# Kernel optimization log

Hardware: AMD Instinct MI355X
Metric: run time of the kernel (lower is better)

## Reference

```python
import jax, jax.numpy as jnp
import numpy as np

B, T, N_X, N_U, N_Y, H = 2048, 2048, 4, 2, 1, 64
MIN_X = jnp.array([0.0, 0.0, 0.0, -jnp.inf], dtype=jnp.float32)
MAX_X = jnp.array([10.0, 10.0, 10.0, jnp.inf], dtype=jnp.float32)
MIN_Y = jnp.array([0.0], dtype=jnp.float32)
MAX_Y = jnp.array([10.0], dtype=jnp.float32)


def setup_inputs() -> dict:
    key = jax.random.key(0)
    ks = jax.random.split(key, 6)
    return {
        "x_0": jax.random.uniform(ks[0], (B, N_X), dtype=jnp.float32) * 5.0,
        "u": jax.random.normal(ks[1], (B, T, N_U), dtype=jnp.float32),
        "theta_f": jnp.array([0.1925, 0.2429, 0.1697, 0.0444, 0.1642], dtype=jnp.float32),
        "theta_h": jnp.zeros((1,), dtype=jnp.float32),
        "tau_u": jnp.ones((1,), dtype=jnp.float32),
        "tau_y": jnp.ones((1,), dtype=jnp.float32),
        "W1": jax.random.normal(ks[2], (N_X + N_U + 5, H), dtype=jnp.float32) / np.sqrt(N_X + N_U + 5),
        "b1": jnp.zeros((H,), dtype=jnp.float32),
        "W2": jax.random.normal(ks[3], (H, N_X), dtype=jnp.float32) * 0.05,
        "Wh": jax.random.normal(ks[4], (N_X, N_Y), dtype=jnp.float32),
    }


def reference(x_0, u, theta_f, theta_h, tau_u, tau_y, W1, b1, W2, Wh):
    Bc = x_0.shape[0]
    tf = jnp.broadcast_to(theta_f[None, :], (Bc, theta_f.shape[0]))
    scale = tau_u[0] / tau_y[0]

    def f(x, ut):
        feat = jnp.concatenate([x, ut, tf], axis=-1)  # (B, n_x+n_u+5)
        return jnp.tanh(feat @ W1 + b1) @ W2 * scale  # (B, n_x)

    def h(x):
        return x @ Wh + theta_h  # (B, n_y)

    y0 = h(x_0)  # unclamped initial output, as in the torch loop

    def step(carry, ut):
        x_step, y_step = carry
        dx = f(x_step, ut)
        x_raw = x_step + dx
        y_new = jnp.clip(h(x_raw), MIN_Y, MAX_Y)  # y computed from pre-clamp state
        x_new = jnp.clip(x_raw, MIN_X, MAX_X)
        return (x_new, y_new), (x_step, y_step)

    u_t = jnp.moveaxis(u, 1, 0)  # (T, B, n_u)
    _, (xs, ys) = jax.lax.scan(step, (x_0, y0), u_t)
    x = jnp.moveaxis(xs, 0, 1)  # (B, T, n_x)
    y = jnp.moveaxis(ys, 0, 1)  # (B, T, n_y)
    return (x, y)
```

## Files before the change

kernel.cpp:

```cpp
#include <hip/hip_runtime.h>

#define B_SZ 2048
#define T_SZ 2048

using f32x16 = float __attribute__((ext_vector_type(16)));
using f32x2  = float __attribute__((ext_vector_type(2)));

template<int CTRL>
__device__ __forceinline__ float dppf(float v) {
  int r = __builtin_amdgcn_update_dpp(0, __builtin_bit_cast(int, v), CTRL, 0xf, 0xf, true);
  return __builtin_bit_cast(float, r);
}

__device__ __forceinline__ f32x2 pkfma(f32x2 a, f32x2 b, f32x2 c) {
  return __builtin_elementwise_fma(a, b, c);
}

#define SSTR 264
#define SBUF (8 * SSTR)

__global__ __launch_bounds__(256, 1) void sss_kernel(
    const float* __restrict__ x0p, const float* __restrict__ up,
    const float* __restrict__ tfp, const float* __restrict__ thp,
    const float* __restrict__ tup, const float* __restrict__ typ,
    const float* __restrict__ W1p, const float* __restrict__ b1p,
    const float* __restrict__ W2p, const float* __restrict__ Whp,
    float* __restrict__ outp)
{
  __shared__ float stageF[2 * SBUF];

  const int tid  = threadIdx.x;
  const int lane = tid & 63;
  const int wv   = __builtin_amdgcn_readfirstlane((int)(tid >> 6));
  const int grp  = lane >> 4;
  const int sl   = lane & 15;
  const int k    = lane & 3;
  const int b0   = blockIdx.x * 16 + wv * 4;
  const int b    = b0 + grp;

  const float K = 2.8853900817779268f;
  f32x2 w1_01[6], w1_23[6];
#pragma unroll
  for (int r = 0; r < 6; ++r) {
    w1_01[r] = f32x2{W1p[r * 64 + sl]      * K, W1p[r * 64 + sl + 16] * K};
    w1_23[r] = f32x2{W1p[r * 64 + sl + 32] * K, W1p[r * 64 + sl + 48] * K};
  }
  float ccs[4];
#pragma unroll
  for (int i = 0; i < 4; ++i) {
    const int u = sl + 16 * i;
    float t = b1p[u];
#pragma unroll
    for (int q = 0; q < 5; ++q) t = fmaf(tfp[q], W1p[(6 + q) * 64 + u], t);
    ccs[i] = t * K;
  }
  const f32x2 cc01 = f32x2{ccs[0], ccs[1]};
  const f32x2 cc23 = f32x2{ccs[2], ccs[3]};

  const float scale = tup[0] / typ[0];
  f32x2 wAB[4], wCD[4];
#pragma unroll
  for (int i = 0; i < 4; ++i) {
    const float4 w2r = ((const float4*)W2p)[sl + 16 * i];
    float col[4] = {w2r.x * scale, w2r.y * scale, w2r.z * scale, w2r.w * scale};
    wAB[i] = f32x2{col[k], col[k ^ 1]};
    wCD[i] = f32x2{col[k ^ 2], col[k ^ 3]};
  }

  const float whl = Whp[k];
  const float th  = thp[0];

  const float lo = (k == 3) ? -__builtin_inff() : 0.0f;
  const float hi = (k == 3) ?  __builtin_inff() : 10.0f;

  float xlane = x0p[b * 4 + k];
  float x0v = dppf<0x00>(xlane);
  float x1v = dppf<0x55>(xlane);
  float x2v = dppf<0xAA>(xlane);
  float x3v = dppf<0xFF>(xlane);

  float p0 = xlane * whl;
  p0 += dppf<0xB1>(p0);
  p0 += dppf<0x4E>(p0);
  float yv = p0 + th;

  const bool is4 = (sl == 4);

  const int m   = sl;
  const int xr  = lane >> 4;
  const int t0  = m >> 1;
  const int k0  = (2 * m) & 3;
  const int rdoff = t0 * SSTR + wv * 64 + 16 * xr + k0;
  const int yoff  = (lane & 7) * SSTR + wv * 64 + 16 * (lane >> 3) + 4;
  float2* gxp = (float2*)outp + (size_t)(b0 + (lane >> 4)) * (T_SZ * 2) + (lane & 15);
  float*  gyp = outp + (size_t)B_SZ * T_SZ * 4 + (size_t)(b0 + (lane >> 3)) * T_SZ + (lane & 7);

  const f32x16* up16 = (const f32x16*)(up + (size_t)b * (T_SZ * 2));
  f32x16 uch = up16[0];
  const int NC = T_SZ / 8;

  for (int c = 0; c < NC; ++c) {
    const int g = (c + 1 < NC) ? c + 1 : NC - 1;
    const f32x16 unx = up16[g];
    float* sw = &stageF[(c & 1) * SBUF + tid];
#pragma unroll
    for (int jj = 0; jj < 8; ++jj) {
      const float vdata = is4 ? yv : xlane;
      sw[jj * SSTR] = vdata;

      const float u0 = uch[2 * jj];
      const float u1 = uch[2 * jj + 1];
      const f32x2 u0p = f32x2{u0, u0};
      const f32x2 u1p = f32x2{u1, u1};

      const f32x2 b01 = pkfma(u1p, w1_01[5], pkfma(u0p, w1_01[4], cc01));
      const f32x2 b23 = pkfma(u1p, w1_23[5], pkfma(u0p, w1_23[4], cc23));

      const f32x2 x0s = f32x2{x0v, x0v};
      const f32x2 x1s = f32x2{x1v, x1v};
      const f32x2 x2s = f32x2{x2v, x2v};
      const f32x2 x3s = f32x2{x3v, x3v};
      const f32x2 mA01 = pkfma(x1s, w1_01[1], x0s * w1_01[0]);
      const f32x2 mB01 = pkfma(x3s, w1_01[3], x2s * w1_01[2]);
      const f32x2 a01  = (b01 + mA01) + mB01;
      const f32x2 mA23 = pkfma(x1s, w1_23[1], x0s * w1_23[0]);
      const f32x2 mB23 = pkfma(x3s, w1_23[3], x2s * w1_23[2]);
      const f32x2 a23  = (b23 + mA23) + mB23;

      float h[4];
      {
        const float av[4] = {a01[0], a01[1], a23[0], a23[1]};
#pragma unroll
        for (int i = 0; i < 4; ++i) {
          const float e  = __builtin_amdgcn_exp2f(av[i]);
          const float rr = __builtin_amdgcn_rcpf(e + 1.0f);
          h[i] = fmaf(-2.0f, rr, 1.0f);
        }
      }
      const f32x2 h0s = f32x2{h[0], h[0]};
      const f32x2 h1s = f32x2{h[1], h[1]};
      const f32x2 h2s = f32x2{h[2], h[2]};
      const f32x2 h3s = f32x2{h[3], h[3]};

      f32x2 qAB = h0s * wAB[0];
      qAB = pkfma(h1s, wAB[1], qAB);
      qAB = pkfma(h2s, wAB[2], qAB);
      qAB = pkfma(h3s, wAB[3], qAB);
      f32x2 qCD = h0s * wCD[0];
      qCD = pkfma(h1s, wCD[1], qCD);
      qCD = pkfma(h2s, wCD[2], qCD);
      qCD = pkfma(h3s, wCD[3], qCD);

      float v = (qAB[0] + dppf<0xB1>(qAB[1]))
              + (dppf<0x4E>(qCD[0]) + dppf<0x1B>(qCD[1]));
      v += dppf<0x124>(v);
      v += dppf<0x128>(v);

      const float w = xlane + v;
      xlane = __builtin_amdgcn_fmed3f(w, lo, hi);

      float p = w * whl;
      p += dppf<0xB1>(p);
      p += dppf<0x4E>(p);
      yv = __builtin_amdgcn_fmed3f(p + th, 0.0f, 10.0f);

      x0v = dppf<0x00>(xlane);
      x1v = dppf<0x55>(xlane);
      x2v = dppf<0xAA>(xlane);
      x3v = dppf<0xFF>(xlane);
    }
    {
      const int bb = (c & 1) * SBUF;
      const float2 xv = *(const float2*)&stageF[bb + rdoff];
      *gxp = xv;
      if (lane < 32) {
        const float yy = stageF[bb + yoff];
        *gyp = yy;
      }
      gxp += 16;
      gyp += 8;
    }
    uch = unx;
  }
}

extern "C" void kernel_launch(void* const* d_in, const int* in_sizes, int n_in,
                              void* d_out, int out_size, void* d_ws, size_t ws_size,
                              hipStream_t stream) {
  (void)in_sizes; (void)n_in; (void)out_size; (void)d_ws; (void)ws_size;
  sss_kernel<<<dim3(B_SZ / 16), dim3(256), 0, stream>>>(
      (const float*)d_in[0], (const float*)d_in[1], (const float*)d_in[2],
      (const float*)d_in[3], (const float*)d_in[4], (const float*)d_in[5],
      (const float*)d_in[6], (const float*)d_in[7], (const float*)d_in[8],
      (const float*)d_in[9], (float*)d_out);
}
```

Baseline: 340.9 us.

## Interleave two batch recurrences per wave and fold tanh constant into state

Each wave now advances two independent batch rows in lockstep so the serial dependency chain of one row can overlap with the other, halving the grid size. The tanh expression is rewritten as 1-2r so the constant term from W2 is precomputed into an offset added to the state, removing per-step multiply-adds, and the cross-lane reduction uses a tree form. The cost is higher register pressure, doubled shared staging, and fewer blocks, which may leave CUs with less wave-level parallelism.

```diff
diff --git a/kernel.cpp b/kernel.cpp
--- a/kernel.cpp
+++ b/kernel.cpp
@@ -27,7 +27,7 @@
     const float* __restrict__ W2p, const float* __restrict__ Whp,
     float* __restrict__ outp)
 {
-  __shared__ float stageF[2 * SBUF];
+  __shared__ float stageF[4 * SBUF];
 
   const int tid  = threadIdx.x;
   const int lane = tid & 63;
@@ -35,8 +35,9 @@
   const int grp  = lane >> 4;
   const int sl   = lane & 15;
   const int k    = lane & 3;
-  const int b0   = blockIdx.x * 16 + wv * 4;
-  const int b    = b0 + grp;
+  const int b0   = blockIdx.x * 32 + wv * 8;
+  const int bA   = b0 + grp;
+  const int bB   = b0 + 4 + grp;
 
   const float K = 2.8853900817779268f;
   f32x2 w1_01[6], w1_23[6];
@@ -67,22 +68,31 @@
     wCD[i] = f32x2{col[k ^ 2], col[k ^ 3]};
   }
 
+  {
+  }
+  const f32x2 oAB = (wAB[0] + wAB[1]) + (wAB[2] + wAB[3]);
+  const f32x2 oCD = (wCD[0] + wCD[1]) + (wCD[2] + wCD[3]);
+  float Cq = (oAB[0] + dppf<0xB1>(oAB[1])) + (dppf<0x4E>(oCD[0]) + dppf<0x1B>(oCD[1]));
+  const float Ck = (Cq + dppf<0x124>(Cq)) + (dppf<0x128>(Cq) + dppf<0x12C>(Cq));
+
   const float whl = Whp[k];
   const float th  = thp[0];
-
   const float lo = (k == 3) ? -__builtin_inff() : 0.0f;
   const float hi = (k == 3) ?  __builtin_inff() : 10.0f;
 
-  float xlane = x0p[b * 4 + k];
-  float x0v = dppf<0x00>(xlane);
-  float x1v = dppf<0x55>(xlane);
-  float x2v = dppf<0xAA>(xlane);
-  float x3v = dppf<0xFF>(xlane);
-
-  float p0 = xlane * whl;
-  p0 += dppf<0xB1>(p0);
-  p0 += dppf<0x4E>(p0);
-  float yv = p0 + th;
+  float xlaneA = x0p[bA * 4 + k];
+  float x0vA = dppf<0x00>(xlaneA), x1vA = dppf<0x55>(xlaneA);
+  float x2vA = dppf<0xAA>(xlaneA), x3vA = dppf<0xFF>(xlaneA);
+  float xCA = xlaneA + Ck;
+  float pA0 = xlaneA * whl; pA0 += dppf<0xB1>(pA0); pA0 += dppf<0x4E>(pA0);
+  float yvA = pA0 + th;
+
+  float xlaneB = x0p[bB * 4 + k];
+  float x0vB = dppf<0x00>(xlaneB), x1vB = dppf<0x55>(xlaneB);
+  float x2vB = dppf<0xAA>(xlaneB), x3vB = dppf<0xFF>(xlaneB);
+  float xCB = xlaneB + Ck;
+  float pB0 = xlaneB * whl; pB0 += dppf<0xB1>(pB0); pB0 += dppf<0x4E>(pB0);
+  float yvB = pB0 + th;
 
   const bool is4 = (sl == 4);
 
@@ -92,95 +102,118 @@
   const int k0  = (2 * m) & 3;
   const int rdoff = t0 * SSTR + wv * 64 + 16 * xr + k0;
   const int yoff  = (lane & 7) * SSTR + wv * 64 + 16 * (lane >> 3) + 4;
-  float2* gxp = (float2*)outp + (size_t)(b0 + (lane >> 4)) * (T_SZ * 2) + (lane & 15);
-  float*  gyp = outp + (size_t)B_SZ * T_SZ * 4 + (size_t)(b0 + (lane >> 3)) * T_SZ + (lane & 7);
-
-  const f32x16* up16 = (const f32x16*)(up + (size_t)b * (T_SZ * 2));
-  f32x16 uch = up16[0];
+  float2* gxpA = (float2*)outp + (size_t)(b0 + (lane >> 4)) * (T_SZ * 2) + (lane & 15);
+  float*  gypA = outp + (size_t)B_SZ * T_SZ * 4 + (size_t)(b0 + (lane >> 3)) * T_SZ + (lane & 7);
+  float2* gxpB = (float2*)outp + (size_t)(b0 + 4 + (lane >> 4)) * (T_SZ * 2) + (lane & 15);
+  float*  gypB = outp + (size_t)B_SZ * T_SZ * 4 + (size_t)(b0 + 4 + (lane >> 3)) * T_SZ + (lane & 7);
+
+  const f32x16* up16A = (const f32x16*)(up + (size_t)bA * (T_SZ * 2));
+  const f32x16* up16B = (const f32x16*)(up + (size_t)bB * (T_SZ * 2));
+  f32x16 uchA = up16A[0];
+  f32x16 uchB = up16B[0];
   const int NC = T_SZ / 8;
 
   for (int c = 0; c < NC; ++c) {
     const int g = (c + 1 < NC) ? c + 1 : NC - 1;
-    const f32x16 unx = up16[g];
-    float* sw = &stageF[(c & 1) * SBUF + tid];
+    const f32x16 unxA = up16A[g];
+    const f32x16 unxB = up16B[g];
+    float* swA = &stageF[((c & 1) * 2 + 0) * SBUF + tid];
+    float* swB = &stageF[((c & 1) * 2 + 1) * SBUF + tid];
 #pragma unroll
     for (int jj = 0; jj < 8; ++jj) {
-      const float vdata = is4 ? yv : xlane;
-      sw[jj * SSTR] = vdata;
-
-      const float u0 = uch[2 * jj];
-      const float u1 = uch[2 * jj + 1];
-      const f32x2 u0p = f32x2{u0, u0};
-      const f32x2 u1p = f32x2{u1, u1};
-
-      const f32x2 b01 = pkfma(u1p, w1_01[5], pkfma(u0p, w1_01[4], cc01));
-      const f32x2 b23 = pkfma(u1p, w1_23[5], pkfma(u0p, w1_23[4], cc23));
-
-      const f32x2 x0s = f32x2{x0v, x0v};
-      const f32x2 x1s = f32x2{x1v, x1v};
-      const f32x2 x2s = f32x2{x2v, x2v};
-      const f32x2 x3s = f32x2{x3v, x3v};
-      const f32x2 mA01 = pkfma(x1s, w1_01[1], x0s * w1_01[0]);
-      const f32x2 mB01 = pkfma(x3s, w1_01[3], x2s * w1_01[2]);
-      const f32x2 a01  = (b01 + mA01) + mB01;
-      const f32x2 mA23 = pkfma(x1s, w1_23[1], x0s * w1_23[0]);
-      const f32x2 mB23 = pkfma(x3s, w1_23[3], x2s * w1_23[2]);
-      const f32x2 a23  = (b23 + mA23) + mB23;
-
-      float h[4];
+      const float vdA = is4 ? yvA : xlaneA;
+      swA[jj * SSTR] = vdA;
+      const float vdB = is4 ? yvB : xlaneB;
+      swB[jj * SSTR] = vdB;
+
+      const float u0A = uchA[2 * jj], u1A = uchA[2 * jj + 1];
+      const float u0B = uchB[2 * jj], u1B = uchB[2 * jj + 1];
+      const f32x2 bA01 = pkfma(f32x2{u1A, u1A}, w1_01[5], pkfma(f32x2{u0A, u0A}, w1_01[4], cc01));
+      const f32x2 bB01 = pkfma(f32x2{u1B, u1B}, w1_01[5], pkfma(f32x2{u0B, u0B}, w1_01[4], cc01));
+      const f32x2 bA23 = pkfma(f32x2{u1A, u1A}, w1_23[5], pkfma(f32x2{u0A, u0A}, w1_23[4], cc23));
+      const f32x2 bB23 = pkfma(f32x2{u1B, u1B}, w1_23[5], pkfma(f32x2{u0B, u0B}, w1_23[4], cc23));
+
+      const f32x2 x0sA = f32x2{x0vA, x0vA}, x1sA = f32x2{x1vA, x1vA};
+      const f32x2 x2sA = f32x2{x2vA, x2vA}, x3sA = f32x2{x3vA, x3vA};
+      const f32x2 x0sB = f32x2{x0vB, x0vB}, x1sB = f32x2{x1vB, x1vB};
+      const f32x2 x2sB = f32x2{x2vB, x2vB}, x3sB = f32x2{x3vB, x3vB};
+      const f32x2 mA01A = pkfma(x1sA, w1_01[1], x0sA * w1_01[0]);
+      const f32x2 mA01B = pkfma(x1sB, w1_01[1], x0sB * w1_01[0]);
+      const f32x2 mB01A = pkfma(x3sA, w1_01[3], x2sA * w1_01[2]);
+      const f32x2 mB01B = pkfma(x3sB, w1_01[3], x2sB * w1_01[2]);
+      const f32x2 aA01 = (mA01A + mB01A) + bA01;
+      const f32x2 aB01 = (mA01B + mB01B) + bB01;
+      const f32x2 mA23A = pkfma(x1sA, w1_23[1], x0sA * w1_23[0]);
+      const f32x2 mA23B = pkfma(x1sB, w1_23[1], x0sB * w1_23[0]);
+      const f32x2 mB23A = pkfma(x3sA, w1_23[3], x2sA * w1_23[2]);
+      const f32x2 mB23B = pkfma(x3sB, w1_23[3], x2sB * w1_23[2]);
+      const f32x2 aA23 = (mA23A + mB23A) + bA23;
+      const f32x2 aB23 = (mA23B + mB23B) + bB23;
+
+      float rA[4], rB[4];
       {
-        const float av[4] = {a01[0], a01[1], a23[0], a23[1]};
+        const float avA[4] = {aA01[0], aA01[1], aA23[0], aA23[1]};
+        const float avB[4] = {aB01[0], aB01[1], aB23[0], aB23[1]};
 #pragma unroll
         for (int i = 0; i < 4; ++i) {
-          const float e  = __builtin_amdgcn_exp2f(av[i]);
-          const float rr = __builtin_amdgcn_rcpf(e + 1.0f);
-          h[i] = fmaf(-2.0f, rr, 1.0f);
+          const float eA = __builtin_amdgcn_exp2f(avA[i]);
+          const float eB = __builtin_amdgcn_exp2f(avB[i]);
+          rA[i] = __builtin_amdgcn_rcpf(eA + 1.0f);
+          rB[i] = __builtin_amdgcn_rcpf(eB + 1.0f);
         }
       }
-      const f32x2 h0s = f32x2{h[0], h[0]};
-      const f32x2 h1s = f32x2{h[1], h[1]};
-      const f32x2 h2s = f32x2{h[2], h[2]};
-      const f32x2 h3s = f32x2{h[3], h[3]};
-
-      f32x2 qAB = h0s * wAB[0];
-      qAB = pkfma(h1s, wAB[1], qAB);
-      qAB = pkfma(h2s, wAB[2], qAB);
-      qAB = pkfma(h3s, wAB[3], qAB);
-      f32x2 qCD = h0s * wCD[0];
-      qCD = pkfma(h1s, wCD[1], qCD);
-      qCD = pkfma(h2s, wCD[2], qCD);
-      qCD = pkfma(h3s, wCD[3], qCD);
-
-      float v = (qAB[0] + dppf<0xB1>(qAB[1]))
-              + (dppf<0x4E>(qCD[0]) + dppf<0x1B>(qCD[1]));
-      v += dppf<0x124>(v);
-      v += dppf<0x128>(v);
-
-      const float w = xlane + v;
-      xlane = __builtin_amdgcn_fmed3f(w, lo, hi);
-
-      float p = w * whl;
-      p += dppf<0xB1>(p);
-      p += dppf<0x4E>(p);
-      yv = __builtin_amdgcn_fmed3f(p + th, 0.0f, 10.0f);
-
-      x0v = dppf<0x00>(xlane);
-      x1v = dppf<0x55>(xlane);
-      x2v = dppf<0xAA>(xlane);
-      x3v = dppf<0xFF>(xlane);
+
+      const f32x2 qABA = pkfma(f32x2{rA[1], rA[1]}, wAB[1], f32x2{rA[0], rA[0]} * wAB[0])
+                       + pkfma(f32x2{rA[3], rA[3]}, wAB[3], f32x2{rA[2], rA[2]} * wAB[2]);
+      const f32x2 qABB = pkfma(f32x2{rB[1], rB[1]}, wAB[1], f32x2{rB[0], rB[0]} * wAB[0])
+                       + pkfma(f32x2{rB[3], rB[3]}, wAB[3], f32x2{rB[2], rB[2]} * wAB[2]);
+      const f32x2 qCDA = pkfma(f32x2{rA[1], rA[1]}, wCD[1], f32x2{rA[0], rA[0]} * wCD[0])
+                       + pkfma(f32x2{rA[3], rA[3]}, wCD[3], f32x2{rA[2], rA[2]} * wCD[2]);
+      const f32x2 qCDB = pkfma(f32x2{rB[1], rB[1]}, wCD[1], f32x2{rB[0], rB[0]} * wCD[0])
+                       + pkfma(f32x2{rB[3], rB[3]}, wCD[3], f32x2{rB[2], rB[2]} * wCD[2]);
+
+      const float vA = (qABA[0] + dppf<0xB1>(qABA[1]))
+                     + (dppf<0x4E>(qCDA[0]) + dppf<0x1B>(qCDA[1]));
+      const float vB = (qABB[0] + dppf<0xB1>(qABB[1]))
+                     + (dppf<0x4E>(qCDB[0]) + dppf<0x1B>(qCDB[1]));
+      const float VA = (vA + dppf<0x124>(vA)) + (dppf<0x128>(vA) + dppf<0x12C>(vA));
+      const float VB = (vB + dppf<0x124>(vB)) + (dppf<0x128>(vB) + dppf<0x12C>(vB));
+
+      const float wA = fmaf(-2.0f, VA, xCA);
+      const float wB = fmaf(-2.0f, VB, xCB);
+
+      float pA = wA * whl; pA += dppf<0xB1>(pA); pA += dppf<0x4E>(pA);
+      yvA = __builtin_amdgcn_fmed3f(pA + th, 0.0f, 10.0f);
+      float pB = wB * whl; pB += dppf<0xB1>(pB); pB += dppf<0x4E>(pB);
+      yvB = __builtin_amdgcn_fmed3f(pB + th, 0.0f, 10.0f);
+
+      xlaneA = __builtin_amdgcn_fmed3f(wA, lo, hi);
+      xlaneB = __builtin_amdgcn_fmed3f(wB, lo, hi);
+      xCA = xlaneA + Ck;
+      xCB = xlaneB + Ck;
+      x0vA = dppf<0x00>(xlaneA); x0vB = dppf<0x00>(xlaneB);
+      x1vA = dppf<0x55>(xlaneA); x1vB = dppf<0x55>(xlaneB);
+      x2vA = dppf<0xAA>(xlaneA); x2vB = dppf<0xAA>(xlaneB);
+      x3vA = dppf<0xFF>(xlaneA); x3vB = dppf<0xFF>(xlaneB);
     }
     {
-      const int bb = (c & 1) * SBUF;
-      const float2 xv = *(const float2*)&stageF[bb + rdoff];
-      *gxp = xv;
+      const int bbA = ((c & 1) * 2 + 0) * SBUF;
+      const int bbB = ((c & 1) * 2 + 1) * SBUF;
+      const float2 xvA = *(const float2*)&stageF[bbA + rdoff];
+      const float2 xvB = *(const float2*)&stageF[bbB + rdoff];
+      *gxpA = xvA;
+      *gxpB = xvB;
       if (lane < 32) {
-        const float yy = stageF[bb + yoff];
-        *gyp = yy;
+        const float yyA = stageF[bbA + yoff];
+        const float yyB = stageF[bbB + yoff];
+        *gypA = yyA;
+        *gypB = yyB;
       }
-      gxp += 16;
-      gyp += 8;
+      gxpA += 16; gxpB += 16;
+      gypA += 8;  gypB += 8;
     }
-    uch = unx;
+    uchA = unxA;
+    uchB = unxB;
   }
 }
 
@@ -188,7 +221,7 @@
                               void* d_out, int out_size, void* d_ws, size_t ws_size,
                               hipStream_t stream) {
   (void)in_sizes; (void)n_in; (void)out_size; (void)d_ws; (void)ws_size;
-  sss_kernel<<<dim3(B_SZ / 16), dim3(256), 0, stream>>>(
+  sss_kernel<<<dim3(B_SZ / 32), dim3(256), 0, stream>>>(
       (const float*)d_in[0], (const float*)d_in[1], (const float*)d_in[2],
       (const float*)d_in[3], (const float*)d_in[4], (const float*)d_in[5],
       (const float*)d_in[6], (const float*)d_in[7], (const float*)d_in[8],
```

Result: slower. 596.7 us (+75.0%).

## Fold tanh affine terms into constant and restructure output staging

Applied to the files above, without the earlier changes.

Rewrites tanh as 1-2r, so the constant part (sum of W2 columns) is precomputed once per lane into Ck and the per-step update becomes a single fma of -2 times the reduced sum plus x+Ck. This removes a per-unit fma from the serial chain, and the final cross-row reduction is turned into a tree instead of two dependent adds. The LDS staging layout is also changed: stride becomes 268, only five lanes store, and the writeback splits half the wave into float4 x stores and half into y stores. Folding the constant changes the floating-point summation order slightly.

```diff
diff --git a/kernel.cpp b/kernel.cpp
--- a/kernel.cpp
+++ b/kernel.cpp
@@ -16,7 +16,7 @@
   return __builtin_elementwise_fma(a, b, c);
 }
 
-#define SSTR 264
+#define SSTR 268
 #define SBUF (8 * SSTR)
 
 __global__ __launch_bounds__(256, 1) void sss_kernel(
@@ -67,9 +67,13 @@
     wCD[i] = f32x2{col[k ^ 2], col[k ^ 3]};
   }
 
+  const f32x2 oAB = (wAB[0] + wAB[1]) + (wAB[2] + wAB[3]);
+  const f32x2 oCD = (wCD[0] + wCD[1]) + (wCD[2] + wCD[3]);
+  float Cq = (oAB[0] + dppf<0xB1>(oAB[1])) + (dppf<0x4E>(oCD[0]) + dppf<0x1B>(oCD[1]));
+  const float Ck = (Cq + dppf<0x124>(Cq)) + (dppf<0x128>(Cq) + dppf<0x12C>(Cq));
+
   const float whl = Whp[k];
   const float th  = thp[0];
-
   const float lo = (k == 3) ? -__builtin_inff() : 0.0f;
   const float hi = (k == 3) ?  __builtin_inff() : 10.0f;
 
@@ -78,22 +82,23 @@
   float x1v = dppf<0x55>(xlane);
   float x2v = dppf<0xAA>(xlane);
   float x3v = dppf<0xFF>(xlane);
+  float xC  = xlane + Ck;
 
   float p0 = xlane * whl;
   p0 += dppf<0xB1>(p0);
   p0 += dppf<0x4E>(p0);
   float yv = p0 + th;
 
-  const bool is4 = (sl == 4);
+  const bool doSt = (sl < 5);
+  const bool is4  = (sl == 4);
 
-  const int m   = sl;
-  const int xr  = lane >> 4;
-  const int t0  = m >> 1;
-  const int k0  = (2 * m) & 3;
-  const int rdoff = t0 * SSTR + wv * 64 + 16 * xr + k0;
-  const int yoff  = (lane & 7) * SSTR + wv * 64 + 16 * (lane >> 3) + 4;
-  float2* gxp = (float2*)outp + (size_t)(b0 + (lane >> 4)) * (T_SZ * 2) + (lane & 15);
-  float*  gyp = outp + (size_t)B_SZ * T_SZ * 4 + (size_t)(b0 + (lane >> 3)) * T_SZ + (lane & 7);
+  const int fr  = (lane & 31) >> 3;
+  const int fs  = lane & 7;
+  const bool isX = lane < 32;
+  const int rdX = fs * SSTR + wv * 64 + fr * 16;
+  const int rdY = rdX + 4;
+  float4* gxp = (float4*)outp + (size_t)(b0 + fr) * T_SZ + fs;
+  float*  gyp = outp + (size_t)B_SZ * T_SZ * 4 + (size_t)(b0 + fr) * T_SZ + fs;
 
   const f32x16* up16 = (const f32x16*)(up + (size_t)b * (T_SZ * 2));
   f32x16 uch = up16[0];
@@ -106,7 +111,7 @@
 #pragma unroll
     for (int jj = 0; jj < 8; ++jj) {
       const float vdata = is4 ? yv : xlane;
-      sw[jj * SSTR] = vdata;
+      if (doSt) sw[jj * SSTR] = vdata;
 
       const float u0 = uch[2 * jj];
       const float u1 = uch[2 * jj + 1];
@@ -127,43 +132,38 @@
       const f32x2 mB23 = pkfma(x3s, w1_23[3], x2s * w1_23[2]);
       const f32x2 a23  = (b23 + mA23) + mB23;
 
-      float h[4];
+      float r_[4];
       {
         const float av[4] = {a01[0], a01[1], a23[0], a23[1]};
 #pragma unroll
         for (int i = 0; i < 4; ++i) {
           const float e  = __builtin_amdgcn_exp2f(av[i]);
-          const float rr = __builtin_amdgcn_rcpf(e + 1.0f);
-          h[i] = fmaf(-2.0f, rr, 1.0f);
+          r_[i] = __builtin_amdgcn_rcpf(e + 1.0f);
         }
       }
-      const f32x2 h0s = f32x2{h[0], h[0]};
-      const f32x2 h1s = f32x2{h[1], h[1]};
-      const f32x2 h2s = f32x2{h[2], h[2]};
-      const f32x2 h3s = f32x2{h[3], h[3]};
+      const f32x2 r0s = f32x2{r_[0], r_[0]};
+      const f32x2 r1s = f32x2{r_[1], r_[1]};
+      const f32x2 r2s = f32x2{r_[2], r_[2]};
+      const f32x2 r3s = f32x2{r_[3], r_[3]};
 
-      f32x2 qAB = h0s * wAB[0];
-      qAB = pkfma(h1s, wAB[1], qAB);
-      qAB = pkfma(h2s, wAB[2], qAB);
-      qAB = pkfma(h3s, wAB[3], qAB);
-      f32x2 qCD = h0s * wCD[0];
-      qCD = pkfma(h1s, wCD[1], qCD);
-      qCD = pkfma(h2s, wCD[2], qCD);
-      qCD = pkfma(h3s, wCD[3], qCD);
+      const f32x2 qAB = pkfma(r1s, wAB[1], r0s * wAB[0])
+                      + pkfma(r3s, wAB[3], r2s * wAB[2]);
+      const f32x2 qCD = pkfma(r1s, wCD[1], r0s * wCD[0])
+                      + pkfma(r3s, wCD[3], r2s * wCD[2]);
 
-      float v = (qAB[0] + dppf<0xB1>(qAB[1]))
-              + (dppf<0x4E>(qCD[0]) + dppf<0x1B>(qCD[1]));
-      v += dppf<0x124>(v);
-      v += dppf<0x128>(v);
+      const float v = (qAB[0] + dppf<0xB1>(qAB[1]))
+                    + (dppf<0x4E>(qCD[0]) + dppf<0x1B>(qCD[1]));
+      const float V = (v + dppf<0x124>(v)) + (dppf<0x128>(v) + dppf<0x12C>(v));
 
-      const float w = xlane + v;
-      xlane = __builtin_amdgcn_fmed3f(w, lo, hi);
+      const float w = fmaf(-2.0f, V, xC);
 
       float p = w * whl;
       p += dppf<0xB1>(p);
       p += dppf<0x4E>(p);
       yv = __builtin_amdgcn_fmed3f(p + th, 0.0f, 10.0f);
 
+      xlane = __builtin_amdgcn_fmed3f(w, lo, hi);
+      xC = xlane + Ck;
       x0v = dppf<0x00>(xlane);
       x1v = dppf<0x55>(xlane);
       x2v = dppf<0xAA>(xlane);
@@ -171,14 +171,15 @@
     }
     {
       const int bb = (c & 1) * SBUF;
-      const float2 xv = *(const float2*)&stageF[bb + rdoff];
-      *gxp = xv;
-      if (lane < 32) {
-        const float yy = stageF[bb + yoff];
+      if (isX) {
+        const float4 xv = *(const float4*)&stageF[bb + rdX];
+        *gxp = xv;
+        gxp += 8;
+      } else {
+        const float yy = stageF[bb + rdY];
         *gyp = yy;
+        gyp += 8;
       }
-      gxp += 16;
-      gyp += 8;
     }
     uch = unx;
   }
```

Result: slower. 358.8 us (+5.2%).
